# Kernel optimization log

Hardware: AMD Instinct MI355X
Metric: run time of the kernel (lower is better)

Reference implementation:

```python
import jax, jax.numpy as jnp
import numpy as np

B, L, F, E, D, N_OUT, FC = 2048, 100, 64, 256, 256, 3, 128


def _lstm_cell(x, h, c, Wi, Wh, b):
    gates = x @ Wi + h @ Wh + b  # (B, 4H)
    i, f, g, o = jnp.split(gates, 4, axis=-1)
    c_new = jax.nn.sigmoid(f) * c + jax.nn.sigmoid(i) * jnp.tanh(g)
    h_new = jax.nn.sigmoid(o) * jnp.tanh(c_new)
    return h_new, c_new


def setup_inputs() -> dict:
    key = jax.random.key(0)
    ks = jax.random.split(key, 12)
    s = 0.05
    return {
        "x": jax.random.normal(ks[0], (B, L, F), jnp.float32),
        # encoder input-attention (shared across timesteps, as in [layer]*look_back)
        "Wa": jax.random.normal(ks[1], (F + E, F), jnp.float32) * s,
        "ba": jnp.zeros((F,), jnp.float32),
        # encoder LSTM cell
        "Wi": jax.random.normal(ks[2], (F, 4 * E), jnp.float32) * s,
        "Wh": jax.random.normal(ks[3], (E, 4 * E), jnp.float32) * s,
        "be": jnp.zeros((4 * E,), jnp.float32),
        # decoder temporal attention
        "Wd": jax.random.normal(ks[4], (E + D, D), jnp.float32) * s,
        "bd": jnp.zeros((D,), jnp.float32),
        "Wl": jax.random.normal(ks[5], (D, 1), jnp.float32) * s,
        "bl": jnp.zeros((1,), jnp.float32),
        # decoder LSTM cell
        "Wdi": jax.random.normal(ks[6], (E, 4 * D), jnp.float32) * s,
        "Wdh": jax.random.normal(ks[7], (D, 4 * D), jnp.float32) * s,
        "bdec": jnp.zeros((4 * D,), jnp.float32),
        # output head: tanh(D->FC) then tanh(FC->1)
        "Wf": jax.random.normal(ks[8], (D, FC), jnp.float32) * s,
        "bf": jnp.zeros((FC,), jnp.float32),
        "Wo": jax.random.normal(ks[9], (FC, 1), jnp.float32) * s,
        "bo": jnp.zeros((1,), jnp.float32),
    }


def reference(x, Wa, ba, Wi, Wh, be, Wd, bd, Wl, bl, Wdi, Wdh, bdec, Wf, bf, Wo, bo):
    # ---------- encoder: per-timestep input attention + LSTM cell ----------
    x_t = jnp.transpose(x, (1, 0, 2))  # (L, B, F)

    def enc_step(carry, xt):
        h, c = carry
        energies = jnp.tanh(jnp.concatenate([xt, h], axis=1) @ Wa + ba)  # (B, F)
        a = jax.nn.softmax(energies, axis=1)
        enc_in = a * xt  # attended input (B, F)
        h, c = _lstm_cell(enc_in, h, c, Wi, Wh, be)
        return (h, c), h

    h0 = jnp.zeros((B, E), x.dtype)
    c0 = jnp.zeros((B, E), x.dtype)
    _, enc_out = jax.lax.scan(enc_step, (h0, c0), x_t)  # (L, B, E)

    # ---------- decoder: temporal attention over encoder states + LSTM ----------
    h_d = jnp.zeros((B, D), x.dtype)
    c_d = jnp.zeros((B, D), x.dtype)
    outs = []
    for _ in range(N_OUT):  # small fixed output horizon
        con = jnp.broadcast_to(h_d[None, :, :], (L, B, D))
        en = jnp.tanh(jnp.concatenate([enc_out, con], axis=2) @ Wd + bd)  # (L, B, D)
        scores = en @ Wl + bl  # (L, B, 1)
        alpha = jax.nn.softmax(scores, axis=0)  # over time
        ctx = jnp.sum(alpha * enc_out, axis=0)  # (B, E)
        h_d, c_d = _lstm_cell(ctx, h_d, c_d, Wdi, Wdh, bdec)
        fc = jnp.tanh(h_d @ Wf + bf)  # (B, FC)
        outs.append(jnp.tanh(fc @ Wo + bo))  # (B, 1)
    return jnp.concatenate(outs, axis=1)  # (B, n_output)
```

## Files before the change

kernel.cpp:

```cpp
#include <hip/hip_runtime.h>
#include <math.h>

#define BB 2048
#define LL 100
#define FF 64
#define EE 256
#define DD 256
#define NOUT 3

#define COMP(v, i) ((i) == 0 ? (v).x : (i) == 1 ? (v).y : (i) == 2 ? (v).z : (v).w)

typedef unsigned short u16;
typedef unsigned int u32;
typedef __attribute__((ext_vector_type(8))) __bf16 bf16x8;
typedef __attribute__((ext_vector_type(4))) float f32x4;
typedef __attribute__((ext_vector_type(2))) float f32x2;

#define MFMA_(A, B, C) __builtin_amdgcn_mfma_f32_16x16x32_bf16((A), (B), (C), 0, 0, 0)

__device__ __forceinline__ float sigmoidf_(float x) {
    return 1.0f / (1.0f + expf(-x));
}
__device__ __forceinline__ float tanhf_(float x) {
    return 1.0f - 2.0f / (1.0f + expf(2.0f * x));
}
__device__ __forceinline__ u16 f2b_(float f) {
    u32 u = __float_as_uint(f);
    u = (u + 0x7FFFu + ((u >> 16) & 1u)) >> 16;
    return (u16)u;
}
__device__ __forceinline__ float b2f_(u16 b) {
    return __uint_as_float(((u32)b) << 16);
}
__device__ __forceinline__ u32 pack2_(float a, float b) {
    return (u32)f2b_(a) | ((u32)f2b_(b) << 16);
}
__device__ __forceinline__ f32x4 splat4(float b) {
    f32x4 v; v[0] = b; v[1] = b; v[2] = b; v[3] = b; return v;
}
__device__ __forceinline__ void split8(const float* v, uint4& H, uint4& L) {
    u16 h[8], lo[8];
    #pragma unroll
    for (int e = 0; e < 8; ++e) {
        h[e]  = f2b_(v[e]);
        lo[e] = f2b_(v[e] - b2f_(h[e]));
    }
    H = make_uint4((u32)h[0]  | ((u32)h[1]  << 16), (u32)h[2]  | ((u32)h[3]  << 16),
                   (u32)h[4]  | ((u32)h[5]  << 16), (u32)h[6]  | ((u32)h[7]  << 16));
    L = make_uint4((u32)lo[0] | ((u32)lo[1] << 16), (u32)lo[2] | ((u32)lo[3] << 16),
                   (u32)lo[4] | ((u32)lo[5] << 16), (u32)lo[6] | ((u32)lo[7] << 16));
}

#define AF(mt, kt, p, ln) (((((mt) * 10 + (kt)) * 2 + (p)) * 64 + (ln)) * 8)
#define AFX(mt, kt, p, ln) AF(mt, kt, p, (ln) ^ (((ln) >> 4) & 3))
#define AF2(mt, kt, p, ln) (((((mt) * 8 + (kt)) * 2 + (p)) * 64 + (ln)) * 8)

__global__ __launch_bounds__(64) void w_prep(
    const float* __restrict__ Wi, const float* __restrict__ Wh,
    const float* __restrict__ Wa, u16* __restrict__ wp)
{
    const int bid = blockIdx.x;
    const int l   = threadIdx.x;
    const int isA = (bid >= 640);
    const int b2  = isA ? bid - 640 : bid;
    const int nt  = b2 / 10, kt = b2 - nt * 10;
    const int col = nt * 16 + (l & 15);

    float v[8];
    #pragma unroll
    for (int e = 0; e < 8; ++e) {
        const int k = kt * 32 + ((l >> 4) << 3) + e;
        v[e] = isA ? Wa[(size_t)k * 64 + col]
                   : (k < 64 ? Wi[(size_t)k * 1024 + col]
                             : Wh[(size_t)(k - 64) * 1024 + col]);
    }
    uint4 H, L;
    split8(v, H, L);
    *(uint4*)&wp[(size_t)bid * 1024 + (size_t)l * 8]       = H;
    *(uint4*)&wp[(size_t)bid * 1024 + 512 + (size_t)l * 8] = L;
}

__global__ __launch_bounds__(64) void w_prep2(
    const float* __restrict__ Wd, u16* __restrict__ wp)
{
    const int bid = blockIdx.x;
    const int l   = threadIdx.x;
    const int nt  = bid >> 3, kt = bid & 7;
    const int col = nt * 16 + (l & 15);
    float v[8];
    #pragma unroll
    for (int e = 0; e < 8; ++e) {
        const int k = kt * 32 + ((l >> 4) << 3) + e;
        v[e] = Wd[(size_t)k * 256 + col];
    }
    uint4 H, L;
    split8(v, H, L);
    u16* tp = wp + (size_t)(680 + bid) * 1024;
    *(uint4*)&tp[(size_t)l * 8]       = H;
    *(uint4*)&tp[512 + (size_t)l * 8] = L;
}

__global__ __launch_bounds__(1024) void enc_mfma4(
    const float* __restrict__ x,
    const float* __restrict__ ba, const float* __restrict__ be,
    const u16* __restrict__ wp,
    float* __restrict__ enc_out,
    float* __restrict__ hbuf,
    u32* __restrict__ flags)
{
    __shared__ u16   aFrag[20480];
    __shared__ float x_s[32 * 68];
    __shared__ float e_s[32 * 68];
    __shared__ float gate_s[4][32][66];

    const int bid = blockIdx.x;
    const int g   = (bid & 7) | ((bid >> 5) << 3);
    const int p   = (bid >> 3) & 3;
    const int row0 = g * 32;
    const int tid = threadIdx.x;
    const int l   = tid & 63;
    const int w   = tid >> 6;

    for (int v = tid; v < 20480 / 2; v += 1024) ((u32*)aFrag)[v] = 0u;

    const int ntW = (w >> 2) * 16 + p * 4 + (w & 3);
    uint4 BhR[10];
    #pragma unroll
    for (int kt = 0; kt < 10; ++kt)
        BhR[kt] = *(const uint4*)&wp[(size_t)(ntW * 10 + kt) * 1024 + (size_t)l * 8];

    const float be_r = be[(size_t)ntW * 16 + (l & 15)];
    const float ba_r = (w < 8) ? ba[(w & 3) * 16 + (l & 15)] : 0.f;

    float c_state[2] = {0.f, 0.f};

    __syncthreads();

    for (int t = 0; t < LL; ++t) {
        if (tid < 256) {
            const int kt2 = tid >> 7;
            const int mt  = (tid >> 6) & 1;
            const int l2  = tid & 63;
            const int row2 = mt * 16 + (l2 & 15);
            const int f0   = kt2 * 32 + ((l2 >> 4) << 3);
            const float* xp = x + (size_t)(row0 + row2) * (LL * FF) + (size_t)t * FF + f0;
            float4 xa = *(const float4*)xp;
            float4 xb = *(const float4*)(xp + 4);
            float v[8] = {xa.x, xa.y, xa.z, xa.w, xb.x, xb.y, xb.z, xb.w};
            uint4 H, L;
            split8(v, H, L);
            *(uint4*)&aFrag[AFX(mt, kt2, 0, l2)] = H;
            *(uint4*)&aFrag[AFX(mt, kt2, 1, l2)] = L;
            *(float4*)&x_s[row2 * 68 + f0]     = xa;
            *(float4*)&x_s[row2 * 68 + f0 + 4] = xb;
        } else if (tid == 1023 && t > 0) {
            const u32 target = 4u * (u32)t;
            int guard = 0;
            while (__hip_atomic_load(&flags[g * 32], __ATOMIC_RELAXED,
                                     __HIP_MEMORY_SCOPE_AGENT) < target) {
                __builtin_amdgcn_s_sleep(1);
                if (++guard > 2000000) break;
            }
        }
        __syncthreads();

        if (t > 0 && tid >= 256) {
            const int v   = tid - 256;
            const int prl = v >> 8;
            const int vv  = v & 255;
            const int row = vv >> 3;
            const int i8  = vv & 7;
            const int ugp = (p + 1 + prl) & 3;
            const int u8  = ugp * 64 + i8 * 8;
            const float* hp_g = hbuf + ((size_t)((t - 1) & 1) * BB + row0 + row) * 256 + u8;
            f32x4 a4, b4;
            asm volatile("global_load_dwordx4 %0, %2, off sc0 sc1\n\t"
                         "global_load_dwordx4 %1, %3, off sc0 sc1\n\t"
                         "s_waitcnt vmcnt(0)"
                         : "=v"(a4), "=v"(b4)
                         : "v"(hp_g), "v"(hp_g + 4) : "memory");
            float v8[8] = {a4[0], a4[1], a4[2], a4[3], b4[0], b4[1], b4[2], b4[3]};
            uint4 H, L;
            split8(v8, H, L);
            const int mt = row >> 4, rowT = row & 15;
            const int kt_h = 2 + (u8 >> 5);
            const int g2   = (u8 & 31) >> 3;
            const int ln   = rowT + (g2 << 4);
            *(uint4*)&aFrag[AFX(mt, kt_h, 0, ln)] = H;
            *(uint4*)&aFrag[AFX(mt, kt_h, 1, ln)] = L;
        }
        __syncthreads();

        if (w < 8) {
            const int mt  = w >> 2;
            const int nta = w & 3;
            f32x4 ea = splat4(ba_r);
            #pragma unroll
            for (int kt = 0; kt < 10; ++kt) {
                bf16x8 Ah = *(const bf16x8*)&aFrag[AFX(mt, kt, 0, l)];
                bf16x8 Al = *(const bf16x8*)&aFrag[AFX(mt, kt, 1, l)];
                const size_t o = (size_t)(640 + nta * 10 + kt) * 1024 + (size_t)l * 8;
                bf16x8 Bh = *(const bf16x8*)&wp[o];
                bf16x8 Bl = *(const bf16x8*)&wp[o + 512];
                ea = MFMA_(Ah, Bh, ea);
                ea = MFMA_(Al, Bh, ea);
                ea = MFMA_(Ah, Bl, ea);
            }
            const int colA = nta * 16 + (l & 15);
            #pragma unroll
            for (int r = 0; r < 4; ++r) {
                const int rowT = ((l >> 4) << 2) + r;
                e_s[(mt * 16 + rowT) * 68 + colA] = tanhf_(ea[r]);
            }
        }
        __syncthreads();

        if (tid < 512) {
            const int row2 = tid >> 4;
            const int c4   = (tid & 15) * 4;
            float4 ev = *(const float4*)&e_s[row2 * 68 + c4];
            float m = fmaxf(fmaxf(ev.x, ev.y), fmaxf(ev.z, ev.w));
            #pragma unroll
            for (int msk = 8; msk >= 1; msk >>= 1) m = fmaxf(m, __shfl_xor(m, msk, 64));
            float4 ex;
            ex.x = expf(ev.x - m); ex.y = expf(ev.y - m);
            ex.z = expf(ev.z - m); ex.w = expf(ev.w - m);
            float s = ex.x + ex.y + ex.z + ex.w;
            #pragma unroll
            for (int msk = 8; msk >= 1; msk >>= 1) s += __shfl_xor(s, msk, 64);
            const float inv = 1.f / s;
            float4 xv = *(const float4*)&x_s[row2 * 68 + c4];
            float ein[4] = { ex.x * inv * xv.x, ex.y * inv * xv.y,
                             ex.z * inv * xv.z, ex.w * inv * xv.w };
            const int mt   = row2 >> 4;
            const int rowT = row2 & 15;
            const int kt   = c4 >> 5;
            const int g2   = (c4 & 31) >> 3;
            const int e0   = c4 & 7;
            const int ln   = rowT + (g2 << 4);
            ushort4 h4, l4;
            #pragma unroll
            for (int e = 0; e < 4; ++e) {
                u16 hh = f2b_(ein[e]);
                u16 ll = f2b_(ein[e] - b2f_(hh));
                if (e == 0) { h4.x = hh; l4.x = ll; } else if (e == 1) { h4.y = hh; l4.y = ll; }
                else if (e == 2) { h4.z = hh; l4.z = ll; } else { h4.w = hh; l4.w = ll; }
            }
            *(ushort4*)&aFrag[AFX(mt, kt, 0, ln) + e0] = h4;
            *(ushort4*)&aFrag[AFX(mt, kt, 1, ln) + e0] = l4;
        }
        __syncthreads();

        f32x4 acc0 = splat4(be_r), acc1 = splat4(be_r);
        #pragma unroll
        for (int kt = 0; kt < 10; ++kt) {
            bf16x8 Ah0 = *(const bf16x8*)&aFrag[AFX(0, kt, 0, l)];
            bf16x8 Al0 = *(const bf16x8*)&aFrag[AFX(0, kt, 1, l)];
            bf16x8 Ah1 = *(const bf16x8*)&aFrag[AFX(1, kt, 0, l)];
            bf16x8 Al1 = *(const bf16x8*)&aFrag[AFX(1, kt, 1, l)];
            bf16x8 Bl  = *(const bf16x8*)&wp[(size_t)(ntW * 10 + kt) * 1024 + 512 + (size_t)l * 8];
            bf16x8 Bh  = __builtin_bit_cast(bf16x8, BhR[kt]);
            acc0 = MFMA_(Ah0, Bh, acc0);
            acc1 = MFMA_(Ah1, Bh, acc1);
            acc0 = MFMA_(Al0, Bh, acc0);
            acc1 = MFMA_(Al1, Bh, acc1);
            acc0 = MFMA_(Ah0, Bl, acc0);
            acc1 = MFMA_(Ah1, Bl, acc1);
        }
        {
            const int gate = w >> 2;
            const int ulb  = (w & 3) * 16 + (l & 15);
            #pragma unroll
            for (int r = 0; r < 4; ++r) {
                const int rT = ((l >> 4) << 2) + r;
                gate_s[gate][rT][ulb]      = acc0[r];
                gate_s[gate][16 + rT][ulb] = acc1[r];
            }
        }
        __syncthreads();

        {
            const int row = tid >> 5;
            const int q2  = (tid & 31) * 2;
            float2 gi2 = *(const float2*)&gate_s[0][row][q2];
            float2 gf2 = *(const float2*)&gate_s[1][row][q2];
            float2 gg2 = *(const float2*)&gate_s[2][row][q2];
            float2 go2 = *(const float2*)&gate_s[3][row][q2];
            float cv0 = sigmoidf_(gf2.x) * c_state[0] + sigmoidf_(gi2.x) * tanhf_(gg2.x);
            float cv1 = sigmoidf_(gf2.y) * c_state[1] + sigmoidf_(gi2.y) * tanhf_(gg2.y);
            c_state[0] = cv0; c_state[1] = cv1;
            float hv0 = sigmoidf_(go2.x) * tanhf_(cv0);
            float hv1 = sigmoidf_(go2.y) * tanhf_(cv1);
            const int u_g = p * 64 + q2;
            *(float2*)&enc_out[((size_t)t * BB + row0 + row) * 256 + u_g]
                = make_float2(hv0, hv1);
            float* hp_g = hbuf + ((size_t)(t & 1) * BB + row0 + row) * 256 + u_g;
            f32x2 hv2; hv2[0] = hv0; hv2[1] = hv1;
            asm volatile("global_store_dwordx2 %0, %1, off sc0 sc1"
                         :: "v"(hp_g), "v"(hv2) : "memory");
            const int mt = row >> 4, rowT = row & 15;
            const int kt_h = 2 + (u_g >> 5);
            const int g2   = (u_g & 31) >> 3;
            const int ln   = rowT + (g2 << 4);
            const int e    = u_g & 7;
            ((u32*)aFrag)[(AFX(mt, kt_h, 0, ln) + e) >> 1] = pack2_(hv0, hv1);
            u16 h0 = f2b_(hv0), h1 = f2b_(hv1);
            ((u32*)aFrag)[(AFX(mt, kt_h, 1, ln) + e) >> 1] =
                (u32)f2b_(hv0 - b2f_(h0)) | ((u32)f2b_(hv1 - b2f_(h1)) << 16);
        }
        asm volatile("s_waitcnt vmcnt(0)" ::: "memory");
        __syncthreads();
        if (tid == 0)
            __hip_atomic_fetch_add(&flags[g * 32], 1u, __ATOMIC_RELEASE,
                                   __HIP_MEMORY_SCOPE_AGENT);
    }
}

__global__ __launch_bounds__(256) void gemm_ep_mfma(
    const float* __restrict__ A, const u16* __restrict__ wp,
    float* __restrict__ C)
{
    __shared__ u16   aF[2 * 8 * 2 * 64 * 8];
    __shared__ float c_s[32 * 260];
    const int m0  = blockIdx.x * 32;
    const int tid = threadIdx.x;
    const int l   = tid & 63;
    const int w   = tid >> 6;

    for (int s = tid; s < 1024; s += 256) {
        const int mt = s >> 9, kt = (s >> 6) & 7, l2 = s & 63;
        const int row2 = mt * 16 + (l2 & 15);
        const int k0   = kt * 32 + ((l2 >> 4) << 3);
        const float* ap = A + (size_t)(m0 + row2) * 256 + k0;
        float4 xa = *(const float4*)ap;
        float4 xb = *(const float4*)(ap + 4);
        float v[8] = {xa.x, xa.y, xa.z, xa.w, xb.x, xb.y, xb.z, xb.w};
        uint4 H, L;
        split8(v, H, L);
        *(uint4*)&aF[AF2(mt, kt, 0, l2)] = H;
        *(uint4*)&aF[AF2(mt, kt, 1, l2)] = L;
    }
    __syncthreads();

    f32x4 acc[2][4];
    #pragma unroll
    for (int mt = 0; mt < 2; ++mt)
        #pragma unroll
        for (int j = 0; j < 4; ++j) acc[mt][j] = splat4(0.f);

    #pragma unroll
    for (int kt = 0; kt < 8; ++kt) {
        bf16x8 Ah0 = *(const bf16x8*)&aF[AF2(0, kt, 0, l)];
        bf16x8 Al0 = *(const bf16x8*)&aF[AF2(0, kt, 1, l)];
        bf16x8 Ah1 = *(const bf16x8*)&aF[AF2(1, kt, 0, l)];
        bf16x8 Al1 = *(const bf16x8*)&aF[AF2(1, kt, 1, l)];
        #pragma unroll
        for (int j = 0; j < 4; ++j) {
            const int nt = w * 4 + j;
            const u16* bt = wp + (size_t)(680 + nt * 8 + kt) * 1024 + (size_t)l * 8;
            bf16x8 Bh = *(const bf16x8*)bt;
            bf16x8 Bl = *(const bf16x8*)(bt + 512);
            acc[0][j] = MFMA_(Ah0, Bh, acc[0][j]);
            acc[1][j] = MFMA_(Ah1, Bh, acc[1][j]);
            acc[0][j] = MFMA_(Al0, Bh, acc[0][j]);
            acc[1][j] = MFMA_(Al1, Bh, acc[1][j]);
            acc[0][j] = MFMA_(Ah0, Bl, acc[0][j]);
            acc[1][j] = MFMA_(Ah1, Bl, acc[1][j]);
        }
    }

    #pragma unroll
    for (int mt = 0; mt < 2; ++mt)
        #pragma unroll
        for (int j = 0; j < 4; ++j) {
            const int col = (w * 4 + j) * 16 + (l & 15);
            #pragma unroll
            for (int r = 0; r < 4; ++r) {
                const int row = mt * 16 + ((l >> 4) << 2) + r;
                c_s[row * 260 + col] = acc[mt][j][r];
            }
        }
    __syncthreads();
    for (int v = tid; v < 32 * 64; v += 256) {
        const int row = v >> 6, c4 = (v & 63) << 2;
        *(float4*)&C[(size_t)(m0 + row) * 256 + c4] = *(const float4*)&c_s[row * 260 + c4];
    }
}

__global__ __launch_bounds__(256) void gemm_nk256(
    const float* __restrict__ A, const float* __restrict__ W,
    const float* __restrict__ bias, float* __restrict__ C, int skip_gemm)
{
    __shared__ float a_s[32 * 256];
    const int m0   = blockIdx.x * 32;
    const int tid  = threadIdx.x;
    const int lane = tid & 63;
    const int rg   = tid >> 6;
    const int n0   = lane * 4;

    float4 bias4 = make_float4(0.f, 0.f, 0.f, 0.f);
    if (bias) bias4 = *(const float4*)&bias[n0];

    if (skip_gemm) {
        #pragma unroll
        for (int r = 0; r < 8; ++r)
            *(float4*)&C[(size_t)(m0 + rg * 8 + r) * 256 + n0] = bias4;
        return;
    }

    for (int v = tid; v < 32 * 64; v += 256)
        ((float4*)a_s)[v] = ((const float4*)(A + (size_t)m0 * 256))[v];
    __syncthreads();

    float4 acc[8];
    #pragma unroll
    for (int r = 0; r < 8; ++r) acc[r] = bias4;

    #pragma unroll 2
    for (int k = 0; k < 256; k += 4) {
        float4 wv[4];
        #pragma unroll
        for (int kk = 0; kk < 4; ++kk)
            wv[kk] = *(const float4*)&W[(size_t)(k + kk) * 256 + n0];
        float4 av[8];
        #pragma unroll
        for (int r = 0; r < 8; ++r)
            av[r] = *(const float4*)&a_s[(rg * 8 + r) * 256 + k];
        #pragma unroll
        for (int kk = 0; kk < 4; ++kk) {
            #pragma unroll
            for (int r = 0; r < 8; ++r) {
                float e = COMP(av[r], kk);
                acc[r].x += e * wv[kk].x; acc[r].y += e * wv[kk].y;
                acc[r].z += e * wv[kk].z; acc[r].w += e * wv[kk].w;
            }
        }
    }
    #pragma unroll
    for (int r = 0; r < 8; ++r)
        *(float4*)&C[(size_t)(m0 + rg * 8 + r) * 256 + n0] = acc[r];
}

__global__ __launch_bounds__(256) void pack_ep(
    float* A, const float* __restrict__ W, u16* epOut, int packed)
{
    __shared__ float a_s[32 * 256];
    const int m0   = blockIdx.x * 32;
    const int tid  = threadIdx.x;
    const int lane = tid & 63;
    const int rg   = tid >> 6;
    const int n0   = lane * 4;

    for (int v = tid; v < 32 * 64; v += 256)
        ((float4*)a_s)[v] = ((const float4*)(A + (size_t)m0 * 256))[v];
    __syncthreads();

    float4 acc[8];
    #pragma unroll
    for (int r = 0; r < 8; ++r) acc[r] = make_float4(0.f, 0.f, 0.f, 0.f);

    #pragma unroll 2
    for (int k = 0; k < 256; k += 4) {
        float4 wv[4];
        #pragma unroll
        for (int kk = 0; kk < 4; ++kk)
            wv[kk] = *(const float4*)&W[(size_t)(k + kk) * 256 + n0];
        float4 av[8];
        #pragma unroll
        for (int r = 0; r < 8; ++r)
            av[r] = *(const float4*)&a_s[(rg * 8 + r) * 256 + k];
        #pragma unroll
        for (int kk = 0; kk < 4; ++kk) {
            #pragma unroll
            for (int r = 0; r < 8; ++r) {
                float e = COMP(av[r], kk);
                acc[r].x += e * wv[kk].x; acc[r].y += e * wv[kk].y;
                acc[r].z += e * wv[kk].z; acc[r].w += e * wv[kk].w;
            }
        }
    }

    u16* epu = packed ? (u16*)A : epOut;
    #pragma unroll
    for (int r = 0; r < 8; ++r) {
        const size_t row = (size_t)(m0 + rg * 8 + r);
        ushort4 o;
        o.x = f2b_(acc[r].x); o.y = f2b_(acc[r].y);
        o.z = f2b_(acc[r].z); o.w = f2b_(acc[r].w);
        u16* dst = packed ? (epu + row * 512 + 256 + n0)
                          : (epu + row * 256 + n0);
        *(ushort4*)dst = o;
    }

    if (packed) {
        u32* ab = (u32*)A;
        for (int v = tid; v < 32 * 128; v += 256) {
            const int row = v >> 7, j = v & 127;
            float2 f = *(const float2*)&a_s[(row << 8) + (j << 1)];
            ab[((size_t)(m0 + row)) * 256 + j] = pack2_(f.x, f.y);
        }
    }
}

__global__ __launch_bounds__(256) void scores_ep_f32(
    const float* __restrict__ ep, const float* __restrict__ hp,
    const float* __restrict__ Wl, float* __restrict__ scores)
{
    __shared__ float hp_s[8 * 256];
    const int b0  = blockIdx.x * 8;
    const int l0  = blockIdx.y * 20;
    const int tid = threadIdx.x;
    const int r   = tid >> 5;
    const int g   = tid & 31;

    for (int v = tid; v < 512; v += 256)
        ((float4*)hp_s)[v] = ((const float4*)(hp + (size_t)b0 * 256))[v];
    __syncthreads();

    const float4 wl0 = *(const float4*)&Wl[g * 4];
    const float4 wl1 = *(const float4*)&Wl[128 + g * 4];
    const float4 h0  = *(const float4*)&hp_s[r * 256 + g * 4];
    const float4 h1  = *(const float4*)&hp_s[r * 256 + 128 + g * 4];
    const float* eb  = ep + (size_t)l0 * (BB * 256) + (size_t)(b0 + r) * 256;

    #pragma unroll 2
    for (int li = 0; li < 20; ++li) {
        float4 e0 = *(const float4*)&eb[(size_t)li * (BB * 256) + g * 4];
        float4 e1 = *(const float4*)&eb[(size_t)li * (BB * 256) + 128 + g * 4];
        float p = tanhf_(e0.x + h0.x) * wl0.x + tanhf_(e0.y + h0.y) * wl0.y
                + tanhf_(e0.z + h0.z) * wl0.z + tanhf_(e0.w + h0.w) * wl0.w
                + tanhf_(e1.x + h1.x) * wl1.x + tanhf_(e1.y + h1.y) * wl1.y
                + tanhf_(e1.z + h1.z) * wl1.z + tanhf_(e1.w + h1.w) * wl1.w;
        #pragma unroll
        for (int msk = 16; msk >= 1; msk >>= 1) p += __shfl_xor(p, msk, 64);
        if (g == 0) scores[(size_t)(l0 + li) * BB + b0 + r] = p;
    }
}

__global__ __launch_bounds__(256) void scores_ep_b16(
    const u16* __restrict__ ep, const float* __restrict__ hp,
    const float* __restrict__ Wl, float* __restrict__ scores,
    int sstr, int soff)
{
    __shared__ float hp_s[8 * 256];
    const int b0  = blockIdx.x * 8;
    const int l0  = blockIdx.y * 20;
    const int tid = threadIdx.x;
    const int r   = tid >> 5;
    const int g   = tid & 31;

    for (int v = tid; v < 512; v += 256)
        ((float4*)hp_s)[v] = ((const float4*)(hp + (size_t)b0 * 256))[v];
    __syncthreads();

    const float4 wl0 = *(const float4*)&Wl[g * 4];
    const float4 wl1 = *(const float4*)&Wl[128 + g * 4];
    const float4 h0  = *(const float4*)&hp_s[r * 256 + g * 4];
    const float4 h1  = *(const float4*)&hp_s[r * 256 + 128 + g * 4];

    #pragma unroll 2
    for (int li = 0; li < 20; ++li) {
        const u16* er = ep + ((size_t)(l0 + li) * BB + b0 + r) * sstr + soff;
        ushort4 u0 = *(const ushort4*)&er[g * 4];
        ushort4 u1 = *(const ushort4*)&er[128 + g * 4];
        float p = tanhf_(b2f_(u0.x) + h0.x) * wl0.x + tanhf_(b2f_(u0.y) + h0.y) * wl0.y
                + tanhf_(b2f_(u0.z) + h0.z) * wl0.z + tanhf_(b2f_(u0.w) + h0.w) * wl0.w
                + tanhf_(b2f_(u1.x) + h1.x) * wl1.x + tanhf_(b2f_(u1.y) + h1.y) * wl1.y
                + tanhf_(b2f_(u1.z) + h1.z) * wl1.z + tanhf_(b2f_(u1.w) + h1.w) * wl1.w;
        #pragma unroll
        for (int msk = 16; msk >= 1; msk >>= 1) p += __shfl_xor(p, msk, 64);
        if (g == 0) scores[(size_t)(l0 + li) * BB + b0 + r] = p;
    }
}

__global__ __launch_bounds__(256) void softmax_ctx(
    const float* __restrict__ scores, const float* __restrict__ enc_out,
    float* __restrict__ ctx)
{
    __shared__ float al_s[8 * 100];
    const int b0  = blockIdx.x * 8;
    const int tid = threadIdx.x;
    for (int v = tid; v < 800; v += 256) {
        int r = v / 100, l = v - r * 100;
        al_s[r * 100 + l] = scores[(size_t)l * BB + b0 + r];
    }
    __syncthreads();
    if (tid < 8) {
        float m = -1e30f;
        for (int l = 0; l < LL; ++l) m = fmaxf(m, al_s[tid * 100 + l]);
        float s = 0.f;
        for (int l = 0; l < LL; ++l) { float e = expf(al_s[tid * 100 + l] - m); al_s[tid * 100 + l] = e; s += e; }
        float inv = 1.f / s;
        for (int l = 0; l < LL; ++l) al_s[tid * 100 + l] *= inv;
    }
    __syncthreads();
    float acc[8] = {};
    for (int l = 0; l < LL; ++l) {
        const float* er = enc_out + (size_t)l * (BB * 256) + (size_t)b0 * 256 + tid;
        #pragma unroll
        for (int r = 0; r < 8; ++r) acc[r] += al_s[r * 100 + l] * er[r * 256];
    }
    for (int r = 0; r < 8; ++r) ctx[(size_t)(b0 + r) * 256 + tid] = acc[r];
}

__global__ __launch_bounds__(256) void softmax_ctx_b16(
    const float* __restrict__ scores, const u16* __restrict__ encp,
    float* __restrict__ ctx)
{
    __shared__ float al_s[8 * 100];
    const int b0  = blockIdx.x * 8;
    const int tid = threadIdx.x;
    for (int v = tid; v < 800; v += 256) {
        int r = v / 100, l = v - r * 100;
        al_s[r * 100 + l] = scores[(size_t)l * BB + b0 + r];
    }
    __syncthreads();
    if (tid < 8) {
        float m = -1e30f;
        for (int l = 0; l < LL; ++l) m = fmaxf(m, al_s[tid * 100 + l]);
        float s = 0.f;
        for (int l = 0; l < LL; ++l) { float e = expf(al_s[tid * 100 + l] - m); al_s[tid * 100 + l] = e; s += e; }
        float inv = 1.f / s;
        for (int l = 0; l < LL; ++l) al_s[tid * 100 + l] *= inv;
    }
    __syncthreads();
    float acc[8] = {};
    for (int l = 0; l < LL; ++l) {
        const u16* er = encp + ((size_t)l * BB + b0) * 512 + tid;
        #pragma unroll
        for (int r = 0; r < 8; ++r) acc[r] += al_s[r * 100 + l] * b2f_(er[r * 512]);
    }
    for (int r = 0; r < 8; ++r) ctx[(size_t)(b0 + r) * 256 + tid] = acc[r];
}

__global__ __launch_bounds__(512) void dec_step(
    const float* __restrict__ ctxp,
    const float* __restrict__ Wdi, const float* __restrict__ Wdh,
    const float* __restrict__ bdec,
    float* __restrict__ hd, float* __restrict__ c_st, int first)
{
    __shared__ float ct_s[8 * 256];
    __shared__ float hd_s[8 * 256];
    __shared__ float gate_s[2][8 * 1024];
    const int row0 = blockIdx.x * 8;
    const int tid  = threadIdx.x;
    const int lane = tid & 63, w = tid >> 6;
    const int half = tid >> 8;
    const int ct   = tid & 255;
    const int c0   = ct * 4;

    ((float4*)ct_s)[tid] = ((const float4*)(ctxp + (size_t)row0 * 256))[tid];
    if (!first)
        ((float4*)hd_s)[tid] = ((const float4*)(hd + (size_t)row0 * 256))[tid];
    __syncthreads();

    float4 acc[8];
    {
        float4 b4 = *(const float4*)&bdec[c0];
        float4 bias4 = (half == 0) ? b4 : make_float4(0.f, 0.f, 0.f, 0.f);
        #pragma unroll
        for (int r = 0; r < 8; ++r) acc[r] = bias4;
    }
    if (half == 0) {
        const float* wP = Wdi + c0;
        #pragma unroll 2
        for (int ch = 0; ch < 64; ++ch) {
            const int k0 = ch * 4;
            float4 w0 = *(const float4*)&wP[(size_t)(k0 + 0) * 1024];
            float4 w1 = *(const float4*)&wP[(size_t)(k0 + 1) * 1024];
            float4 w2 = *(const float4*)&wP[(size_t)(k0 + 2) * 1024];
            float4 w3 = *(const float4*)&wP[(size_t)(k0 + 3) * 1024];
            #pragma unroll
            for (int r = 0; r < 8; ++r) {
                float4 av = *(const float4*)&ct_s[r * 256 + k0];
                acc[r].x += av.x * w0.x; acc[r].y += av.x * w0.y;
                acc[r].z += av.x * w0.z; acc[r].w += av.x * w0.w;
                acc[r].x += av.y * w1.x; acc[r].y += av.y * w1.y;
                acc[r].z += av.y * w1.z; acc[r].w += av.y * w1.w;
                acc[r].x += av.z * w2.x; acc[r].y += av.z * w2.y;
                acc[r].z += av.z * w2.z; acc[r].w += av.z * w2.w;
                acc[r].x += av.w * w3.x; acc[r].y += av.w * w3.y;
                acc[r].z += av.w * w3.z; acc[r].w += av.w * w3.w;
            }
        }
    } else if (!first) {
        const float* wP = Wdh + c0;
        #pragma unroll 2
        for (int ch = 0; ch < 64; ++ch) {
            const int k0 = ch * 4;
            float4 w0 = *(const float4*)&wP[(size_t)(k0 + 0) * 1024];
            float4 w1 = *(const float4*)&wP[(size_t)(k0 + 1) * 1024];
            float4 w2 = *(const float4*)&wP[(size_t)(k0 + 2) * 1024];
            float4 w3 = *(const float4*)&wP[(size_t)(k0 + 3) * 1024];
            #pragma unroll
            for (int r = 0; r < 8; ++r) {
                float4 av = *(const float4*)&hd_s[r * 256 + k0];
                acc[r].x += av.x * w0.x; acc[r].y += av.x * w0.y;
                acc[r].z += av.x * w0.z; acc[r].w += av.x * w0.w;
                acc[r].x += av.y * w1.x; acc[r].y += av.y * w1.y;
                acc[r].z += av.y * w1.z; acc[r].w += av.y * w1.w;
                acc[r].x += av.z * w2.x; acc[r].y += av.z * w2.y;
                acc[r].z += av.z * w2.z; acc[r].w += av.z * w2.w;
                acc[r].x += av.w * w3.x; acc[r].y += av.w * w3.y;
                acc[r].z += av.w * w3.z; acc[r].w += av.w * w3.w;
            }
        }
    }
    #pragma unroll
    for (int r = 0; r < 8; ++r)
        *(float4*)&gate_s[half][r * 1024 + c0] = acc[r];
    __syncthreads();

    {
        const float* g0 = &gate_s[0][w * 1024 + lane * 4];
        const float* g1 = &gate_s[1][w * 1024 + lane * 4];
        float4 giA = *(const float4*)&g0[0],   giB = *(const float4*)&g1[0];
        float4 gfA = *(const float4*)&g0[256], gfB = *(const float4*)&g1[256];
        float4 ggA = *(const float4*)&g0[512], ggB = *(const float4*)&g1[512];
        float4 goA = *(const float4*)&g0[768], goB = *(const float4*)&g1[768];
        size_t ci = (size_t)(row0 + w) * 256 + lane * 4;
        float4 c4 = first ? make_float4(0.f, 0.f, 0.f, 0.f)
                          : *(const float4*)&c_st[ci];
        float cc[4] = { c4.x, c4.y, c4.z, c4.w };
        float gi[4] = { giA.x + giB.x, giA.y + giB.y, giA.z + giB.z, giA.w + giB.w };
        float gf[4] = { gfA.x + gfB.x, gfA.y + gfB.y, gfA.z + gfB.z, gfA.w + gfB.w };
        float gg[4] = { ggA.x + ggB.x, ggA.y + ggB.y, ggA.z + ggB.z, ggA.w + ggB.w };
        float go[4] = { goA.x + goB.x, goA.y + goB.y, goA.z + goB.z, goA.w + goB.w };
        float4 cn, hn;
        #pragma unroll
        for (int uu = 0; uu < 4; ++uu) {
            float cv = sigmoidf_(gf[uu]) * cc[uu] + sigmoidf_(gi[uu]) * tanhf_(gg[uu]);
            float hv = sigmoidf_(go[uu]) * tanhf_(cv);
            if (uu == 0) { cn.x = cv; hn.x = hv; } else if (uu == 1) { cn.y = cv; hn.y = hv; }
            else if (uu == 2) { cn.z = cv; hn.z = hv; } else { cn.w = cv; hn.w = hv; }
        }
        *(float4*)&c_st[ci] = cn;
        *(float4*)&hd[ci]   = hn;
    }
}

__global__ __launch_bounds__(256) void head_k(
    const float* __restrict__ hd, const float* __restrict__ Wf,
    const float* __restrict__ bf, const float* __restrict__ Wo,
    const float* __restrict__ bo, float* __restrict__ out, int step)
{
    __shared__ float hd_s[16 * 256];
    __shared__ float fc_s[16 * 128];
    const int b0  = blockIdx.x * 16;
    const int tid = threadIdx.x;
    {
        const float4* hg = (const float4*)(hd + (size_t)b0 * 256);
        for (int i = tid; i < 1024; i += 256) ((float4*)hd_s)[i] = hg[i];
    }
    __syncthreads();
    {
        const int f = tid & 127, rg = tid >> 7;
        float acc[8];
        float bfv = bf[f];
        #pragma unroll
        for (int rr = 0; rr < 8; ++rr) acc[rr] = bfv;
        const float* wp = Wf + f;
        #pragma unroll 2
        for (int k = 0; k < 256; ++k) {
            float wv = wp[k * 128];
            #pragma unroll
            for (int rr = 0; rr < 8; ++rr) acc[rr] += hd_s[(rg * 8 + rr) * 256 + k] * wv;
        }
        for (int rr = 0; rr < 8; ++rr) fc_s[(rg * 8 + rr) * 128 + f] = tanhf_(acc[rr]);
    }
    __syncthreads();
    {
        const int lane = tid & 63, w = tid >> 6;
        const float bov = bo[0];
        #pragma unroll
        for (int rr = 0; rr < 4; ++rr) {
            int r = w * 4 + rr;
            float p = fc_s[r * 128 + lane] * Wo[lane] + fc_s[r * 128 + 64 + lane] * Wo[64 + lane];
            #pragma unroll
            for (int msk = 32; msk >= 1; msk >>= 1) p += __shfl_xor(p, msk, 64);
            if (lane == 0) out[(size_t)(b0 + r) * NOUT + step] = tanhf_(p + bov);
        }
    }
}

extern "C" void kernel_launch(void* const* d_in, const int* in_sizes, int n_in,
                              void* d_out, int out_size, void* d_ws, size_t ws_size,
                              hipStream_t stream)
{
    const float* x    = (const float*)d_in[0];
    const float* Wa   = (const float*)d_in[1];
    const float* ba   = (const float*)d_in[2];
    const float* Wi   = (const float*)d_in[3];
    const float* Wh   = (const float*)d_in[4];
    const float* be   = (const float*)d_in[5];
    const float* Wd   = (const float*)d_in[6];
    const float* bd   = (const float*)d_in[7];
    const float* Wl   = (const float*)d_in[8];
    const float* bl   = (const float*)d_in[9];
    const float* Wdi  = (const float*)d_in[10];
    const float* Wdh  = (const float*)d_in[11];
    const float* bdec = (const float*)d_in[12];
    const float* Wf   = (const float*)d_in[13];
    const float* bf   = (const float*)d_in[14];
    const float* Wo   = (const float*)d_in[15];
    const float* bo   = (const float*)d_in[16];
    float* out = (float*)d_out;

    const size_t f_enc    = (size_t)LL * BB * EE;
    const size_t f_state  = (size_t)BB * EE;
    const size_t f_scores = (size_t)LL * BB;
    const size_t need3 = (f_enc + 3 * f_state + f_scores) * sizeof(float);
    const size_t need2 = need3 + f_enc * sizeof(u16);
    const size_t need1 = need3 + f_enc * sizeof(float);

    float* ws      = (float*)d_ws;
    float* enc_out = ws;
    float* hd      = enc_out + f_enc;
    float* c_d     = hd + f_state;
    float* ctx     = c_d + f_state;
    float* scores  = ctx + f_state;
    float* ep32    = scores + f_scores;
    u16*   ep16    = (u16*)(scores + f_scores);
    float* hp      = ctx;
    u16*   wprep   = (u16*)ctx;
    float* hbuf    = hd;
    u32*   flags   = (u32*)scores;

    if (ws_size < need3) return;
    const int tier = (ws_size >= need1) ? 1 : (ws_size >= need2) ? 2 : 3;

    hipMemsetAsync(flags, 0, 64 * 32 * sizeof(u32), stream);
    w_prep<<<680, 64, 0, stream>>>(Wi, Wh, Wa, wprep);
    w_prep2<<<128, 64, 0, stream>>>(Wd, wprep);
    enc_mfma4<<<256, 1024, 0, stream>>>(x, ba, be, wprep, enc_out, hbuf, flags);

    if (tier == 1)
        gemm_ep_mfma<<<(LL * BB) / 32, 256, 0, stream>>>(enc_out, wprep, ep32);
    else
        pack_ep<<<(LL * BB) / 32, 256, 0, stream>>>(
            enc_out, Wd, ep16, tier == 3 ? 1 : 0);

    for (int s = 0; s < NOUT; ++s) {
        gemm_nk256<<<BB / 32, 256, 0, stream>>>(
            hd, Wd + 256 * 256, bd, hp, s == 0);
        if (tier == 1)
            scores_ep_f32<<<dim3(BB / 8, 5), 256, 0, stream>>>(ep32, hp, Wl, scores);
        else if (tier == 2)
            scores_ep_b16<<<dim3(BB / 8, 5), 256, 0, stream>>>(ep16, hp, Wl, scores, 256, 0);
        else
            scores_ep_b16<<<dim3(BB / 8, 5), 256, 0, stream>>>(
                (const u16*)enc_out, hp, Wl, scores, 512, 256);
        if (tier == 3)
            softmax_ctx_b16<<<BB / 8, 256, 0, stream>>>(scores, (const u16*)enc_out, ctx);
        else
            softmax_ctx<<<BB / 8, 256, 0, stream>>>(scores, enc_out, ctx);
        dec_step<<<BB / 8, 512, 0, stream>>>(ctx, Wdi, Wdh, bdec, hd, c_d, s == 0);
        head_k<<<BB / 16, 256, 0, stream>>>(hd, Wf, bf, Wo, bo, out, s);
    }
}
```

Before: 2.481 ms.

## Exchange encoder hidden state as pre-split bf16 hi/lo and release flag earlier

The inter-block hidden-state exchange buffer now holds pre-split bf16 hi/lo halves instead of fp32, so consumers load the MFMA fragments directly without re-splitting. The producer computes the split once and reuses it for both the global store and the local fragment. All consumer threads now spin on the flag themselves, which removes a block barrier before the h load. The completion flag is released before the enc_out store and local fragment writes, shortening the critical path of the cross-block recurrence. The trade-off is more threads polling the flag in global memory.

```diff
diff --git a/kernel.cpp b/kernel.cpp
--- a/kernel.cpp
+++ b/kernel.cpp
@@ -14,7 +14,6 @@
 typedef unsigned int u32;
 typedef __attribute__((ext_vector_type(8))) __bf16 bf16x8;
 typedef __attribute__((ext_vector_type(4))) float f32x4;
-typedef __attribute__((ext_vector_type(2))) float f32x2;
 
 #define MFMA_(A, B, C) __builtin_amdgcn_mfma_f32_16x16x32_bf16((A), (B), (C), 0, 0, 0)
 
@@ -105,7 +104,8 @@
     const float* __restrict__ ba, const float* __restrict__ be,
     const u16* __restrict__ wp,
     float* __restrict__ enc_out,
-    float* __restrict__ hbuf,
+    u16* __restrict__ hbh,
+    u16* __restrict__ hbl,
     u32* __restrict__ flags)
 {
     __shared__ u16   aFrag[20480];
@@ -153,7 +153,7 @@
             *(uint4*)&aFrag[AFX(mt, kt2, 1, l2)] = L;
             *(float4*)&x_s[row2 * 68 + f0]     = xa;
             *(float4*)&x_s[row2 * 68 + f0 + 4] = xb;
-        } else if (tid == 1023 && t > 0) {
+        } else if (t > 0) {
             const u32 target = 4u * (u32)t;
             int guard = 0;
             while (__hip_atomic_load(&flags[g * 32], __ATOMIC_RELAXED,
@@ -161,10 +161,6 @@
                 __builtin_amdgcn_s_sleep(1);
                 if (++guard > 2000000) break;
             }
-        }
-        __syncthreads();
-
-        if (t > 0 && tid >= 256) {
             const int v   = tid - 256;
             const int prl = v >> 8;
             const int vv  = v & 255;
@@ -172,16 +168,13 @@
             const int i8  = vv & 7;
             const int ugp = (p + 1 + prl) & 3;
             const int u8  = ugp * 64 + i8 * 8;
-            const float* hp_g = hbuf + ((size_t)((t - 1) & 1) * BB + row0 + row) * 256 + u8;
-            f32x4 a4, b4;
+            const size_t hoff = ((size_t)((t - 1) & 1) * BB + row0 + row) * 256 + u8;
+            uint4 H, L;
             asm volatile("global_load_dwordx4 %0, %2, off sc0 sc1\n\t"
                          "global_load_dwordx4 %1, %3, off sc0 sc1\n\t"
                          "s_waitcnt vmcnt(0)"
-                         : "=v"(a4), "=v"(b4)
-                         : "v"(hp_g), "v"(hp_g + 4) : "memory");
-            float v8[8] = {a4[0], a4[1], a4[2], a4[3], b4[0], b4[1], b4[2], b4[3]};
-            uint4 H, L;
-            split8(v8, H, L);
+                         : "=v"(H), "=v"(L)
+                         : "v"(hbh + hoff), "v"(hbl + hoff) : "memory");
             const int mt = row >> 4, rowT = row & 15;
             const int kt_h = 2 + (u8 >> 5);
             const int g2   = (u8 & 31) >> 3;
@@ -279,9 +272,11 @@
         }
         __syncthreads();
 
+        const int row = tid >> 5;
+        const int q2  = (tid & 31) * 2;
+        float hv0, hv1;
+        u32 hw, lw;
         {
-            const int row = tid >> 5;
-            const int q2  = (tid & 31) * 2;
             float2 gi2 = *(const float2*)&gate_s[0][row][q2];
             float2 gf2 = *(const float2*)&gate_s[1][row][q2];
             float2 gg2 = *(const float2*)&gate_s[2][row][q2];
@@ -289,30 +284,37 @@
             float cv0 = sigmoidf_(gf2.x) * c_state[0] + sigmoidf_(gi2.x) * tanhf_(gg2.x);
             float cv1 = sigmoidf_(gf2.y) * c_state[1] + sigmoidf_(gi2.y) * tanhf_(gg2.y);
             c_state[0] = cv0; c_state[1] = cv1;
-            float hv0 = sigmoidf_(go2.x) * tanhf_(cv0);
-            float hv1 = sigmoidf_(go2.y) * tanhf_(cv1);
+            hv0 = sigmoidf_(go2.x) * tanhf_(cv0);
+            hv1 = sigmoidf_(go2.y) * tanhf_(cv1);
+            const u16 hi0 = f2b_(hv0), hi1 = f2b_(hv1);
+            const u16 lo0 = f2b_(hv0 - b2f_(hi0));
+            const u16 lo1 = f2b_(hv1 - b2f_(hi1));
+            hw = (u32)hi0 | ((u32)hi1 << 16);
+            lw = (u32)lo0 | ((u32)lo1 << 16);
+            const size_t hoff = ((size_t)(t & 1) * BB + row0 + row) * 256 + p * 64 + q2;
+            asm volatile("global_store_dword %0, %2, off sc0 sc1\n\t"
+                         "global_store_dword %1, %3, off sc0 sc1"
+                         :: "v"(hbh + hoff), "v"(hbl + hoff), "v"(hw), "v"(lw)
+                         : "memory");
+        }
+        asm volatile("s_waitcnt vmcnt(0)" ::: "memory");
+        __syncthreads();
+        if (tid == 0)
+            __hip_atomic_fetch_add(&flags[g * 32], 1u, __ATOMIC_RELEASE,
+                                   __HIP_MEMORY_SCOPE_AGENT);
+
+        {
             const int u_g = p * 64 + q2;
             *(float2*)&enc_out[((size_t)t * BB + row0 + row) * 256 + u_g]
                 = make_float2(hv0, hv1);
-            float* hp_g = hbuf + ((size_t)(t & 1) * BB + row0 + row) * 256 + u_g;
-            f32x2 hv2; hv2[0] = hv0; hv2[1] = hv1;
-            asm volatile("global_store_dwordx2 %0, %1, off sc0 sc1"
-                         :: "v"(hp_g), "v"(hv2) : "memory");
             const int mt = row >> 4, rowT = row & 15;
             const int kt_h = 2 + (u_g >> 5);
             const int g2   = (u_g & 31) >> 3;
             const int ln   = rowT + (g2 << 4);
             const int e    = u_g & 7;
-            ((u32*)aFrag)[(AFX(mt, kt_h, 0, ln) + e) >> 1] = pack2_(hv0, hv1);
-            u16 h0 = f2b_(hv0), h1 = f2b_(hv1);
-            ((u32*)aFrag)[(AFX(mt, kt_h, 1, ln) + e) >> 1] =
-                (u32)f2b_(hv0 - b2f_(h0)) | ((u32)f2b_(hv1 - b2f_(h1)) << 16);
-        }
-        asm volatile("s_waitcnt vmcnt(0)" ::: "memory");
-        __syncthreads();
-        if (tid == 0)
-            __hip_atomic_fetch_add(&flags[g * 32], 1u, __ATOMIC_RELEASE,
-                                   __HIP_MEMORY_SCOPE_AGENT);
+            ((u32*)aFrag)[(AFX(mt, kt_h, 0, ln) + e) >> 1] = hw;
+            ((u32*)aFrag)[(AFX(mt, kt_h, 1, ln) + e) >> 1] = lw;
+        }
     }
 }
 
@@ -823,7 +825,8 @@
     u16*   ep16    = (u16*)(scores + f_scores);
     float* hp      = ctx;
     u16*   wprep   = (u16*)ctx;
-    float* hbuf    = hd;
+    u16*   hbh     = (u16*)hd;
+    u16*   hbl     = (u16*)c_d;
     u32*   flags   = (u32*)scores;
 
     if (ws_size < need3) return;
@@ -832,7 +835,7 @@
     hipMemsetAsync(flags, 0, 64 * 32 * sizeof(u32), stream);
     w_prep<<<680, 64, 0, stream>>>(Wi, Wh, Wa, wprep);
     w_prep2<<<128, 64, 0, stream>>>(Wd, wprep);
-    enc_mfma4<<<256, 1024, 0, stream>>>(x, ba, be, wprep, enc_out, hbuf, flags);
+    enc_mfma4<<<256, 1024, 0, stream>>>(x, ba, be, wprep, enc_out, hbh, hbl, flags);
 
     if (tier == 1)
         gemm_ep_mfma<<<(LL * BB) / 32, 256, 0, stream>>>(enc_out, wprep, ep32);
```

After: 2.657 ms. 7.1% more time.
